# Performance work log

Measured on AMD Instinct MI355X. Metric: run time of the kernel, lower is better.

## Reference

```python
import jax, jax.numpy as jnp
import numpy as np

B = 32          # num graphs
N = 4096        # nodes per graph (temporal length after reshape)
TOT = B * N     # 131072 total nodes
F = 64          # num_features
HS = 128        # hidden_dim_s
RS = 32         # rank_s
HT = 128        # hidden_dim_t
RT = 32         # rank_t
E = 1048576     # num edges


def setup_inputs() -> dict:
    key = jax.random.key(0)
    ks = jax.random.split(key, 20)
    x = jax.random.normal(ks[0], (TOT, F), jnp.float32)
    edge_index = jax.random.randint(ks[1], (2, E), 0, TOT, dtype=jnp.int64)
    batch = jnp.repeat(jnp.arange(B, dtype=jnp.int64), N)

    def lin(k, fan_in, fan_out):
        s = 1.0 / np.sqrt(fan_in)
        return jax.random.uniform(k, (fan_in, fan_out), jnp.float32, -s, s)

    def conv(k, cout, cin):
        s = 1.0 / np.sqrt(cin * 3)
        return jax.random.uniform(k, (cout, cin, 3), jnp.float32, -s, s)

    return {
        "x": x, "edge_index": edge_index, "batch": batch,
        "W1": lin(ks[2], F, HS), "b1": jnp.zeros((HS,), jnp.float32),
        "W2": lin(ks[3], HS, RS), "b2": jnp.zeros((RS,), jnp.float32),
        "W3": lin(ks[4], RS, HS), "b3": jnp.zeros((HS,), jnp.float32),
        "tW1": conv(ks[5], HT, HS), "tb1": jnp.zeros((HT,), jnp.float32),
        "tW2": conv(ks[6], RT, HT), "tb2": jnp.zeros((RT,), jnp.float32),
        "tW3": conv(ks[7], HT, RT), "tb3": jnp.zeros((HT,), jnp.float32),
        "Wpi": lin(ks[8], HT, 1), "bpi": jnp.zeros((1,), jnp.float32),
        "Wn": lin(ks[9], HT, 1), "bn": jnp.zeros((1,), jnp.float32),
        "Wp": lin(ks[10], HT, 1), "bp": jnp.zeros((1,), jnp.float32),
    }


def reference(x, edge_index, batch,
              W1, b1, W2, b2, W3, b3,
              tW1, tb1, tW2, tb2, tW3, tb3,
              Wpi, bpi, Wn, bn, Wp, bp):
    src, dst = edge_index[0], edge_index[1]
    n = x.shape[0]

    # GCN symmetric normalization with added self-loops (PyG GCNConv default)
    deg = jnp.zeros((n,), x.dtype).at[dst].add(1.0) + 1.0  # +1 self-loop
    dinv = jax.lax.rsqrt(deg)
    enorm = dinv[src] * dinv[dst]       # [E] edge normalization
    snorm = dinv * dinv                 # [n] self-loop normalization

    def gcn(h, W, b):
        h = h @ W                                            # [n, out]
        agg = jnp.zeros_like(h).at[dst].add(h[src] * enorm[:, None])
        return agg + h * snorm[:, None] + b

    xs = jax.nn.relu(gcn(x, W1, b1))
    xs = jax.nn.relu(gcn(xs, W2, b2))
    xs = jax.nn.relu(gcn(xs, W3, b3))    # [TOT, HS]

    num_graphs = B  # == batch.max() + 1 (batch is repeat(arange(B), N))
    xs = xs.reshape(num_graphs, -1, xs.shape[-1]).transpose(0, 2, 1)  # [B, HS, N]

    def conv1d(z, w, bias):
        y = jax.lax.conv_general_dilated(
            z, w, window_strides=(1,), padding=((1, 1),),
            dimension_numbers=("NCH", "OIH", "NCH"))
        return y + bias[None, :, None]

    xt = jax.nn.relu(conv1d(xs, tW1, tb1))
    xt = jax.nn.relu(conv1d(xt, tW2, tb2))
    xt = jax.nn.relu(conv1d(xt, tW3, tb3))                   # [B, HT, N]

    xt = xt.transpose(0, 2, 1).reshape(-1, xt.shape[1])      # [TOT, HT]

    pi = jax.nn.sigmoid(xt @ Wpi + bpi)
    nb = jax.nn.softplus(xt @ Wn + bn)
    p = jax.nn.sigmoid(xt @ Wp + bp)
    return (pi, nb, p)
```

## Files before the change

kernel.cpp:

```cpp
#include <hip/hip_runtime.h>
#include <cmath>

constexpr int TOT = 131072;
constexpr int NE  = 1048576;
constexpr int NMASK = 4095;

constexpr int NB   = 512;
constexpr int DPB  = 256;
constexpr int BCAP = 4096;
constexpr int EPB  = 2048;

typedef __attribute__((ext_vector_type(8))) short bf16x8;
typedef __attribute__((ext_vector_type(4))) float f32x4;

__device__ inline float bf2f(unsigned int u16) {
    union { unsigned int i; float f; } x; x.i = u16 << 16; return x.f;
}
__device__ inline unsigned short f2bf(float f) {
    union { float f; unsigned int i; } x; x.f = f;
    unsigned int r = (x.i + 0x7fffu + ((x.i >> 16) & 1u)) >> 16;
    return (unsigned short)r;
}
__device__ inline void unpack8(uint4 v, float* f) {
    f[0] = bf2f(v.x & 0xffffu); f[1] = bf2f(v.x >> 16);
    f[2] = bf2f(v.y & 0xffffu); f[3] = bf2f(v.y >> 16);
    f[4] = bf2f(v.z & 0xffffu); f[5] = bf2f(v.z >> 16);
    f[6] = bf2f(v.w & 0xffffu); f[7] = bf2f(v.w >> 16);
}
__device__ inline uint4 pack8(const float* f) {
    uint4 v;
    v.x = (unsigned)f2bf(f[0]) | ((unsigned)f2bf(f[1]) << 16);
    v.y = (unsigned)f2bf(f[2]) | ((unsigned)f2bf(f[3]) << 16);
    v.z = (unsigned)f2bf(f[4]) | ((unsigned)f2bf(f[5]) << 16);
    v.w = (unsigned)f2bf(f[6]) | ((unsigned)f2bf(f[7]) << 16);
    return v;
}

__device__ inline void pack_one(const float* __restrict__ w, unsigned short* __restrict__ wp,
                                int CIN, int COUT, int taps, int idx) {
    int j = idx & 7;
    int L = (idx >> 3) & 63;
    int f = idx >> 9;
    int NT = COUT >> 4;
    int kc = f / NT, nt = f - kc * NT;
    int k = kc * 32 + (L >> 4) * 8 + j;
    int n = nt * 16 + (L & 15);
    float v;
    if (taps == 1) v = w[k * COUT + n];
    else { int t = k / CIN, c = k - t * CIN; v = w[(n * CIN + c) * 3 + t]; }
    wp[idx] = f2bf(v);
}

struct PackArgs {
    const float *W1, *W2, *W3, *tW1, *tW2, *tW3;
    unsigned short *g1, *g2, *g3, *c1, *c2, *c3;
};
__global__ __launch_bounds__(256) void k_part(const int* __restrict__ src,
                                              const int* __restrict__ dst,
                                              int* __restrict__ gcur,
                                              unsigned* __restrict__ buf,
                                              PackArgs pa) {
    __shared__ int hist[NB];
    __shared__ int cbase[NB];
    __shared__ int lcur[NB];
    const int tid = threadIdx.x;
    const int e0 = blockIdx.x * EPB;

    for (int b = tid; b < NB; b += 256) hist[b] = 0;
    __syncthreads();
    for (int i = tid; i < EPB; i += 256)
        atomicAdd(&hist[dst[e0 + i] >> 8], 1);
    __syncthreads();
    for (int b = tid; b < NB; b += 256) {
        int c = hist[b];
        cbase[b] = (c > 0) ? atomicAdd(&gcur[b * 32], c) : 0;
        lcur[b] = 0;
    }
    __syncthreads();
    for (int i = tid; i < EPB; i += 256) {
        int e = e0 + i;
        int d = dst[e];
        int b = d >> 8;
        int p = atomicAdd(&lcur[b], 1);
        buf[b * BCAP + cbase[b] + p] = ((unsigned)src[e] << 8) | (unsigned)(d & 255);
    }
    int gid = blockIdx.x * 256 + tid;
    if      (gid <  8192) pack_one(pa.W1,  pa.g1, 64, 128, 1, gid);
    else if (gid < 12288) pack_one(pa.W2,  pa.g2, 128, 32, 1, gid - 8192);
    else if (gid < 16384) pack_one(pa.W3,  pa.g3, 32, 128, 1, gid - 12288);
    else if (gid < 65536) pack_one(pa.tW1, pa.c1, 128, 128, 3, gid - 16384);
    else if (gid < 77824) pack_one(pa.tW2, pa.c2, 128, 32, 3, gid - 65536);
    else if (gid < 90112) pack_one(pa.tW3, pa.c3, 32, 128, 3, gid - 77824);
}

__global__ __launch_bounds__(256) void k_bcsr(const unsigned* __restrict__ buf,
                                              const int* __restrict__ gcur,
                                              int* __restrict__ adj,
                                              int2* __restrict__ rse,
                                              float* __restrict__ dinv,
                                              const float4* __restrict__ x,
                                              uint4* __restrict__ xsc) {
    __shared__ int cnt[DPB];
    __shared__ int start[DPB];
    __shared__ int cur[DPB];
    __shared__ int sc[DPB];
    const int b = blockIdx.x;
    const int tid = threadIdx.x;
    cnt[tid] = 0;
    __syncthreads();
    const int n = gcur[b * 32];
    const unsigned* eb = buf + b * BCAP;
    for (int i = tid; i < n; i += 256)
        atomicAdd(&cnt[eb[i] & 255u], 1);
    __syncthreads();
    int v = cnt[tid];
    sc[tid] = v;
    __syncthreads();
    for (int off = 1; off < 256; off <<= 1) {
        int a = sc[tid];
        int p = (tid >= off) ? sc[tid - off] : 0;
        __syncthreads();
        sc[tid] = a + p;
        __syncthreads();
    }
    int st = sc[tid] - v;
    start[tid] = st;
    cur[tid] = 0;
    int d = (b << 8) + tid;
    rse[d] = make_int2(b * BCAP + st, v);
    dinv[d] = rsqrtf((float)v + 1.0f);
    __syncthreads();
    for (int i = tid; i < n; i += 256) {
        unsigned w = eb[i];
        int dl = (int)(w & 255u);
        int p = atomicAdd(&cur[dl], 1);
        adj[b * BCAP + start[dl] + p] = (int)(w >> 8);
    }
    for (int i = tid; i < DPB * 8; i += 256) {
        int rl = i >> 3;
        int t = (b << 11) + i;
        float dv = rsqrtf((float)cnt[rl] + 1.0f);
        float4 v0 = x[t * 2], v1 = x[t * 2 + 1];
        float f[8] = { v0.x * dv, v0.y * dv, v0.z * dv, v0.w * dv,
                       v1.x * dv, v1.y * dv, v1.z * dv, v1.w * dv };
        xsc[t] = pack8(f);
    }
}

template<int LC>
__global__ __launch_bounds__(256) void k_gcsr(const uint4* __restrict__ xs,
                                              const int* __restrict__ adj,
                                              const int2* __restrict__ rse,
                                              const float* __restrict__ dinv,
                                              const float* __restrict__ bias,
                                              uint4* __restrict__ out) {
    int t = blockIdx.x * 256 + threadIdx.x;
    int d = t >> LC;
    int g = t & ((1 << LC) - 1);
    float a[8];
    unpack8(xs[t], a);
    int2 se = rse[d];
    int e = se.x, end = se.x + se.y;
    for (; e + 4 <= end; e += 4) {
        int s0 = adj[e], s1 = adj[e + 1], s2 = adj[e + 2], s3 = adj[e + 3];
        uint4 v0 = xs[(s0 << LC) + g];
        uint4 v1 = xs[(s1 << LC) + g];
        uint4 v2 = xs[(s2 << LC) + g];
        uint4 v3 = xs[(s3 << LC) + g];
        float f[8];
        unpack8(v0, f);
#pragma unroll
        for (int j = 0; j < 8; ++j) a[j] += f[j];
        unpack8(v1, f);
#pragma unroll
        for (int j = 0; j < 8; ++j) a[j] += f[j];
        unpack8(v2, f);
#pragma unroll
        for (int j = 0; j < 8; ++j) a[j] += f[j];
        unpack8(v3, f);
#pragma unroll
        for (int j = 0; j < 8; ++j) a[j] += f[j];
    }
    for (; e < end; ++e) {
        float f[8];
        unpack8(xs[(adj[e] << LC) + g], f);
#pragma unroll
        for (int j = 0; j < 8; ++j) a[j] += f[j];
    }
    float dv = dinv[d];
#pragma unroll
    for (int j = 0; j < 8; ++j)
        a[j] = fmaxf(fmaf(a[j], dv, bias[g * 8 + j]), 0.0f) * dv;
    out[t] = pack8(a);
}

__global__ __launch_bounds__(256) void k_gmm2(const uint4* __restrict__ xs,
                                              const int* __restrict__ adj,
                                              const int2* __restrict__ rse,
                                              const float* __restrict__ dinv,
                                              const bf16x8* __restrict__ wp1,
                                              const float* __restrict__ b1,
                                              const bf16x8* __restrict__ wp2,
                                              unsigned short* __restrict__ y) {
    constexpr int CIN = 64;
    constexpr int ROWS = 64;
    constexpr int SC  = CIN + 8;
    constexpr int SCH = 144;
    constexpr int NV = CIN / 8;
    constexpr int VPT = NV / 4;
    __shared__ __attribute__((aligned(16))) unsigned short tile1[ROWS * SC];
    __shared__ __attribute__((aligned(16))) unsigned short h1t[ROWS * SCH];

    const int R0 = blockIdx.x * ROWS;
    const int tid = threadIdx.x;

    {
        int r = R0 + (tid >> 2);
        int g = tid & 3;
        const uint4* base = xs + (long)r * NV + g * VPT;
        float a[VPT * 8];
#pragma unroll
        for (int v = 0; v < VPT; ++v) unpack8(base[v], a + v * 8);
        int2 se = rse[r];
        int e = se.x, end = se.x + se.y;
        for (; e + 4 <= end; e += 4) {
            int s0 = adj[e], s1 = adj[e + 1], s2 = adj[e + 2], s3 = adj[e + 3];
            const uint4* p0 = xs + (long)s0 * NV + g * VPT;
            const uint4* p1 = xs + (long)s1 * NV + g * VPT;
            const uint4* p2 = xs + (long)s2 * NV + g * VPT;
            const uint4* p3 = xs + (long)s3 * NV + g * VPT;
            uint4 v0[VPT], v1[VPT], v2[VPT], v3[VPT];
#pragma unroll
            for (int v = 0; v < VPT; ++v) { v0[v] = p0[v]; v1[v] = p1[v]; v2[v] = p2[v]; v3[v] = p3[v]; }
            float f[VPT * 8];
#pragma unroll
            for (int v = 0; v < VPT; ++v) unpack8(v0[v], f + v * 8);
#pragma unroll
            for (int j = 0; j < VPT * 8; ++j) a[j] += f[j];
#pragma unroll
            for (int v = 0; v < VPT; ++v) unpack8(v1[v], f + v * 8);
#pragma unroll
            for (int j = 0; j < VPT * 8; ++j) a[j] += f[j];
#pragma unroll
            for (int v = 0; v < VPT; ++v) unpack8(v2[v], f + v * 8);
#pragma unroll
            for (int j = 0; j < VPT * 8; ++j) a[j] += f[j];
#pragma unroll
            for (int v = 0; v < VPT; ++v) unpack8(v3[v], f + v * 8);
#pragma unroll
            for (int j = 0; j < VPT * 8; ++j) a[j] += f[j];
        }
        for (; e < end; ++e) {
            const uint4* p0 = xs + (long)adj[e] * NV + g * VPT;
            float f[VPT * 8];
#pragma unroll
            for (int v = 0; v < VPT; ++v) unpack8(p0[v], f + v * 8);
#pragma unroll
            for (int j = 0; j < VPT * 8; ++j) a[j] += f[j];
        }
        float dv = dinv[r];
#pragma unroll
        for (int j = 0; j < VPT * 8; ++j) a[j] *= dv;
        uint4* dst4 = (uint4*)(tile1 + (tid >> 2) * SC + g * VPT * 8);
#pragma unroll
        for (int v = 0; v < VPT; ++v) dst4[v] = pack8(a + v * 8);
    }
    __syncthreads();

    const int lane = tid & 63;
    const int w = tid >> 6;
    const int l16 = lane & 15;
    const int q = lane >> 4;

    {
        f32x4 acc[4][2];
#pragma unroll
        for (int wm = 0; wm < 4; ++wm)
#pragma unroll
            for (int nt = 0; nt < 2; ++nt) acc[wm][nt] = (f32x4){0.f, 0.f, 0.f, 0.f};
        const bf16x8* wpl = wp1 + lane;
        const int nt0 = w * 2;
#pragma unroll
        for (int kc = 0; kc < 2; ++kc) {
            bf16x8 a[4];
#pragma unroll
            for (int wm = 0; wm < 4; ++wm)
                a[wm] = *(const bf16x8*)(tile1 + (wm * 16 + l16) * SC + kc * 32 + q * 8);
            bf16x8 b[2];
#pragma unroll
            for (int nt = 0; nt < 2; ++nt)
                b[nt] = wpl[(kc * 8 + nt0 + nt) * 64];
#pragma unroll
            for (int wm = 0; wm < 4; ++wm)
#pragma unroll
                for (int nt = 0; nt < 2; ++nt)
                    acc[wm][nt] = __builtin_amdgcn_mfma_f32_16x16x32_bf16(a[wm], b[nt], acc[wm][nt], 0, 0, 0);
        }
#pragma unroll
        for (int wm = 0; wm < 4; ++wm) {
#pragma unroll
            for (int nt = 0; nt < 2; ++nt) {
                int col = w * 32 + nt * 16 + l16;
                float bi = b1[col];
#pragma unroll
                for (int r = 0; r < 4; ++r) {
                    int row = wm * 16 + q * 4 + r;
                    h1t[row * SCH + col] = f2bf(fmaxf(acc[wm][nt][r] + bi, 0.0f));
                }
            }
        }
    }
    __syncthreads();

    {
        const int colbase = (w & 1) * 16;
        const int rowbase = (w >> 1) * 32;
        const int nt0 = colbase >> 4;
        f32x4 acc[2];
#pragma unroll
        for (int wm = 0; wm < 2; ++wm) acc[wm] = (f32x4){0.f, 0.f, 0.f, 0.f};
        const bf16x8* wpl = wp2 + lane;
#pragma unroll
        for (int kc = 0; kc < 4; ++kc) {
            bf16x8 a[2];
#pragma unroll
            for (int wm = 0; wm < 2; ++wm)
                a[wm] = *(const bf16x8*)(h1t + (rowbase + wm * 16 + l16) * SCH + kc * 32 + q * 8);
            bf16x8 b = wpl[(kc * 2 + nt0) * 64];
#pragma unroll
            for (int wm = 0; wm < 2; ++wm)
                acc[wm] = __builtin_amdgcn_mfma_f32_16x16x32_bf16(a[wm], b, acc[wm], 0, 0, 0);
        }
#pragma unroll
        for (int wm = 0; wm < 2; ++wm) {
            int col = colbase + l16;
#pragma unroll
            for (int r = 0; r < 4; ++r) {
                int row = R0 + rowbase + wm * 16 + q * 4 + r;
                float v = acc[wm][r] * dinv[row];
                y[(long)row * 32 + col] = f2bf(v);
            }
        }
    }
}

template<int CIN, bool RELU>
__global__ __launch_bounds__(256) void k_gmm(const uint4* __restrict__ xs,
                                             const int* __restrict__ adj,
                                             const int2* __restrict__ rse,
                                             const float* __restrict__ dinv,
                                             const bf16x8* __restrict__ wp,
                                             const float* __restrict__ bias,
                                             unsigned short* __restrict__ y) {
    constexpr int COUT = 128;
    constexpr int ROWS = 64;
    constexpr int SC = CIN + 8;
    constexpr int NV = CIN / 8;
    constexpr int VPT = NV / 4;
    constexpr int NK = CIN / 32;
    constexpr int NT = COUT / 16;
    constexpr int WN = 2, WM = 4;
    __shared__ __attribute__((aligned(16))) unsigned short tile[ROWS * SC];

    const int R0 = blockIdx.x * ROWS;
    const int tid = threadIdx.x;

    {
        int r = R0 + (tid >> 2);
        int g = tid & 3;
        const uint4* base = xs + (long)r * NV + g * VPT;
        float a[VPT * 8];
#pragma unroll
        for (int v = 0; v < VPT; ++v) unpack8(base[v], a + v * 8);
        int2 se = rse[r];
        int e = se.x, end = se.x + se.y;
        for (; e + 4 <= end; e += 4) {
            int s0 = adj[e], s1 = adj[e + 1], s2 = adj[e + 2], s3 = adj[e + 3];
            const uint4* p0 = xs + (long)s0 * NV + g * VPT;
            const uint4* p1 = xs + (long)s1 * NV + g * VPT;
            const uint4* p2 = xs + (long)s2 * NV + g * VPT;
            const uint4* p3 = xs + (long)s3 * NV + g * VPT;
            uint4 v0[VPT], v1[VPT], v2[VPT], v3[VPT];
#pragma unroll
            for (int v = 0; v < VPT; ++v) { v0[v] = p0[v]; v1[v] = p1[v]; v2[v] = p2[v]; v3[v] = p3[v]; }
            float f[VPT * 8];
#pragma unroll
            for (int v = 0; v < VPT; ++v) unpack8(v0[v], f + v * 8);
#pragma unroll
            for (int j = 0; j < VPT * 8; ++j) a[j] += f[j];
#pragma unroll
            for (int v = 0; v < VPT; ++v) unpack8(v1[v], f + v * 8);
#pragma unroll
            for (int j = 0; j < VPT * 8; ++j) a[j] += f[j];
#pragma unroll
            for (int v = 0; v < VPT; ++v) unpack8(v2[v], f + v * 8);
#pragma unroll
            for (int j = 0; j < VPT * 8; ++j) a[j] += f[j];
#pragma unroll
            for (int v = 0; v < VPT; ++v) unpack8(v3[v], f + v * 8);
#pragma unroll
            for (int j = 0; j < VPT * 8; ++j) a[j] += f[j];
        }
        for (; e < end; ++e) {
            const uint4* p0 = xs + (long)adj[e] * NV + g * VPT;
            float f[VPT * 8];
#pragma unroll
            for (int v = 0; v < VPT; ++v) unpack8(p0[v], f + v * 8);
#pragma unroll
            for (int j = 0; j < VPT * 8; ++j) a[j] += f[j];
        }
        float dv = dinv[r];
#pragma unroll
        for (int j = 0; j < VPT * 8; ++j) a[j] *= dv;
        uint4* dst4 = (uint4*)(tile + (tid >> 2) * SC + g * VPT * 8);
#pragma unroll
        for (int v = 0; v < VPT; ++v) dst4[v] = pack8(a + v * 8);
    }
    __syncthreads();

    const int lane = threadIdx.x & 63;
    const int w = threadIdx.x >> 6;
    const int l16 = lane & 15;
    const int q = lane >> 4;
    const int colbase = w * 32;
    const int nt0 = colbase >> 4;

    f32x4 acc[WM][WN];
#pragma unroll
    for (int wm = 0; wm < WM; ++wm)
#pragma unroll
        for (int nt = 0; nt < WN; ++nt) acc[wm][nt] = (f32x4){0.f, 0.f, 0.f, 0.f};

    const bf16x8* __restrict__ wpl = wp + lane;

#pragma unroll
    for (int kc = 0; kc < NK; ++kc) {
        bf16x8 a[WM];
#pragma unroll
        for (int wm = 0; wm < WM; ++wm)
            a[wm] = *(const bf16x8*)(tile + (wm * 16 + l16) * SC + kc * 32 + q * 8);
        bf16x8 b[WN];
#pragma unroll
        for (int nt = 0; nt < WN; ++nt)
            b[nt] = wpl[(kc * NT + nt0 + nt) * 64];
#pragma unroll
        for (int wm = 0; wm < WM; ++wm)
#pragma unroll
            for (int nt = 0; nt < WN; ++nt)
                acc[wm][nt] = __builtin_amdgcn_mfma_f32_16x16x32_bf16(a[wm], b[nt], acc[wm][nt], 0, 0, 0);
    }

#pragma unroll
    for (int wm = 0; wm < WM; ++wm) {
#pragma unroll
        for (int nt = 0; nt < WN; ++nt) {
            int col = colbase + nt * 16 + l16;
            float bi = bias[col];
#pragma unroll
            for (int r = 0; r < 4; ++r) {
                int row = R0 + wm * 16 + q * 4 + r;
                float v = acc[wm][nt][r] + bi;
                if (RELU) v = fmaxf(v, 0.0f);
                y[(long)row * COUT + col] = f2bf(v);
            }
        }
    }
}

template<int CIN, int COUT, int TAPS, bool RELU, bool BIAS, bool SOUT>
__global__ __launch_bounds__(256) void k_mm(const unsigned short* __restrict__ x,
                                            const bf16x8* __restrict__ wp,
                                            const float* __restrict__ bias,
                                            const float* __restrict__ dinv,
                                            unsigned short* __restrict__ y) {
    constexpr int ROWS = 64;
    constexpr int HALO = (TAPS == 3) ? 1 : 0;
    constexpr int TR = ROWS + 2 * HALO;
    constexpr int SC = CIN + 8;
    constexpr int NCH = CIN / 32;
    constexpr int NK = TAPS * NCH;
    constexpr int NT = COUT / 16;
    constexpr int WN = (COUT == 128) ? 2 : 1;
    constexpr int WM = (COUT == 128) ? 4 : 2;
    __shared__ __attribute__((aligned(16))) unsigned short tile[TR * SC];

    const int R0 = blockIdx.x * ROWS;
    const int n0 = R0 & NMASK; (void)n0;

    constexpr int NLD = TR * (CIN / 8);
    for (int idx = threadIdx.x; idx < NLD; idx += 256) {
        int tr = idx / (CIN / 8);
        int c8 = idx - tr * (CIN / 8);
        int ro = tr - HALO;
        bool valid = true;
        if (TAPS == 3) {
            if (ro < 0) valid = (n0 > 0);
            else if (ro >= ROWS) valid = (n0 + ROWS < 4096);
        }
        uint4 v = make_uint4(0, 0, 0, 0);
        if (valid) v = *(const uint4*)(x + (long)(R0 + ro) * CIN + c8 * 8);
        *(uint4*)(tile + tr * SC + c8 * 8) = v;
    }
    __syncthreads();

    const int lane = threadIdx.x & 63;
    const int w = threadIdx.x >> 6;
    const int l16 = lane & 15;
    const int q = lane >> 4;
    const int colbase = (COUT == 128) ? w * 32 : (w & 1) * 16;
    const int rowbase = (COUT == 128) ? 0 : (w >> 1) * 32;
    const int nt0 = colbase >> 4;

    f32x4 acc[WM][WN];
#pragma unroll
    for (int wm = 0; wm < WM; ++wm)
#pragma unroll
        for (int nt = 0; nt < WN; ++nt) acc[wm][nt] = (f32x4){0.f, 0.f, 0.f, 0.f};

    const bf16x8* __restrict__ wpl = wp + lane;

#pragma unroll
    for (int kc = 0; kc < NK; ++kc) {
        const int tap = (TAPS == 3) ? (kc / NCH) : 0;
        const int ch  = (TAPS == 3) ? (kc - tap * NCH) : kc;
        bf16x8 a[WM];
#pragma unroll
        for (int wm = 0; wm < WM; ++wm)
            a[wm] = *(const bf16x8*)(tile + (rowbase + wm * 16 + l16 + tap) * SC + ch * 32 + q * 8);
        bf16x8 b[WN];
#pragma unroll
        for (int nt = 0; nt < WN; ++nt)
            b[nt] = wpl[(kc * NT + nt0 + nt) * 64];
#pragma unroll
        for (int wm = 0; wm < WM; ++wm)
#pragma unroll
            for (int nt = 0; nt < WN; ++nt)
                acc[wm][nt] = __builtin_amdgcn_mfma_f32_16x16x32_bf16(a[wm], b[nt], acc[wm][nt], 0, 0, 0);
    }

#pragma unroll
    for (int wm = 0; wm < WM; ++wm) {
#pragma unroll
        for (int nt = 0; nt < WN; ++nt) {
            int col = colbase + nt * 16 + l16;
            float bi = BIAS ? bias[col] : 0.0f;
#pragma unroll
            for (int r = 0; r < 4; ++r) {
                int row = R0 + rowbase + wm * 16 + q * 4 + r;
                float v = acc[wm][nt][r] + bi;
                if (RELU) v = fmaxf(v, 0.0f);
                if (SOUT) v *= dinv[row];
                y[(long)row * COUT + col] = f2bf(v);
            }
        }
    }
}

__global__ __launch_bounds__(256) void k_c23_heads(
    const unsigned short* __restrict__ x,
    const bf16x8* __restrict__ wp2, const float* __restrict__ tb2,
    const bf16x8* __restrict__ wp3, const float* __restrict__ tb3,
    const float* __restrict__ Wpi, const float* __restrict__ bpi,
    const float* __restrict__ Wn,  const float* __restrict__ bn,
    const float* __restrict__ Wp,  const float* __restrict__ bp,
    float* __restrict__ out) {
    constexpr int SC1 = 136;
    constexpr int SC2 = 40;
    __shared__ __attribute__((aligned(16))) unsigned short shl[82 * 136 + 66 * 40];
    unsigned short* c1  = shl;
    unsigned short* c2  = shl + 82 * 136;
    unsigned short* xts = shl;

    const int R0 = blockIdx.x * 64;
    const int n0 = R0 & NMASK;
    const int tid = threadIdx.x;

    for (int i = tid; i < 82 * 16; i += 256) {
        int r = i >> 4;
        int c8 = i & 15;
        int n = n0 - 2 + r;
        uint4 v = make_uint4(0, 0, 0, 0);
        if (n >= 0 && n < 4096)
            v = *(const uint4*)(x + (long)(R0 - 2 + r) * 128 + c8 * 8);
        *(uint4*)(c1 + r * SC1 + c8 * 8) = v;
    }
    __syncthreads();

    const int lane = tid & 63;
    const int w = tid >> 6;
    const int l16 = lane & 15;
    const int q = lane >> 4;

    for (int rt = w; rt < 5; rt += 4) {
        f32x4 acc[2];
#pragma unroll
        for (int nt = 0; nt < 2; ++nt) acc[nt] = (f32x4){0.f, 0.f, 0.f, 0.f};
        const bf16x8* wpl = wp2 + lane;
#pragma unroll
        for (int kc = 0; kc < 12; ++kc) {
            int tap = kc >> 2, ch = kc & 3;
            bf16x8 a = *(const bf16x8*)(c1 + (16 * rt + l16 + tap) * SC1 + ch * 32 + q * 8);
            bf16x8 b0 = wpl[(kc * 2 + 0) * 64];
            bf16x8 b1 = wpl[(kc * 2 + 1) * 64];
            acc[0] = __builtin_amdgcn_mfma_f32_16x16x32_bf16(a, b0, acc[0], 0, 0, 0);
            acc[1] = __builtin_amdgcn_mfma_f32_16x16x32_bf16(a, b1, acc[1], 0, 0, 0);
        }
#pragma unroll
        for (int nt = 0; nt < 2; ++nt) {
            int col = nt * 16 + l16;
            float bi = tb2[col];
#pragma unroll
            for (int r = 0; r < 4; ++r) {
                int idx = 16 * rt + q * 4 + r;
                if (idx < 66) {
                    int n = n0 - 1 + idx;
                    unsigned short v = 0;
                    if (n >= 0 && n < 4096)
                        v = f2bf(fmaxf(acc[nt][r] + bi, 0.0f));
                    c2[idx * SC2 + col] = v;
                }
            }
        }
    }
    __syncthreads();

    {
        f32x4 acc[4][2];
#pragma unroll
        for (int rt = 0; rt < 4; ++rt)
#pragma unroll
            for (int nt = 0; nt < 2; ++nt) acc[rt][nt] = (f32x4){0.f, 0.f, 0.f, 0.f};
        const bf16x8* wpl = wp3 + lane;
#pragma unroll
        for (int kc = 0; kc < 3; ++kc) {
            bf16x8 a[4];
#pragma unroll
            for (int rt = 0; rt < 4; ++rt)
                a[rt] = *(const bf16x8*)(c2 + (16 * rt + l16 + kc) * SC2 + q * 8);
            bf16x8 b[2];
#pragma unroll
            for (int nt = 0; nt < 2; ++nt)
                b[nt] = wpl[(kc * 8 + 2 * w + nt) * 64];
#pragma unroll
            for (int rt = 0; rt < 4; ++rt)
#pragma unroll
                for (int nt = 0; nt < 2; ++nt)
                    acc[rt][nt] = __builtin_amdgcn_mfma_f32_16x16x32_bf16(a[rt], b[nt], acc[rt][nt], 0, 0, 0);
        }
#pragma unroll
        for (int rt = 0; rt < 4; ++rt) {
#pragma unroll
            for (int nt = 0; nt < 2; ++nt) {
                int col = w * 32 + nt * 16 + l16;
                float bi = tb3[col];
#pragma unroll
                for (int r = 0; r < 4; ++r) {
                    int row = 16 * rt + q * 4 + r;
                    xts[row * 130 + col] = f2bf(fmaxf(acc[rt][nt][r] + bi, 0.0f));
                }
            }
        }
    }
    __syncthreads();

    if (tid < 192) {
        int h = tid >> 6;
        int row = tid & 63;
        const float* Wh = (h == 0) ? Wpi : (h == 1) ? Wn : Wp;
        float s = 0.0f;
        const unsigned short* xr = xts + row * 130;
#pragma unroll
        for (int c2i = 0; c2i < 64; ++c2i) {
            unsigned u = *(const unsigned*)(xr + c2i * 2);
            s = fmaf(bf2f(u & 0xffffu), Wh[c2i * 2], s);
            s = fmaf(bf2f(u >> 16), Wh[c2i * 2 + 1], s);
        }
        float bb = (h == 0) ? bpi[0] : (h == 1) ? bn[0] : bp[0];
        float z = s + bb;
        float o;
        if (h == 1) o = (z > 20.0f) ? z : log1pf(expf(z));
        else        o = 1.0f / (1.0f + expf(-z));
        out[h * TOT + R0 + row] = o;
    }
}

extern "C" void kernel_launch(void* const* d_in, const int* in_sizes, int n_in,
                              void* d_out, int out_size, void* d_ws, size_t ws_size,
                              hipStream_t stream) {
    const float* x   = (const float*)d_in[0];
    const int*   ei  = (const int*)d_in[1];
    const int*   src = ei;
    const int*   dst = ei + NE;
    const float* W1 = (const float*)d_in[3];
    const float* b1 = (const float*)d_in[4];
    const float* W2 = (const float*)d_in[5];
    const float* b2 = (const float*)d_in[6];
    const float* W3 = (const float*)d_in[7];
    const float* b3 = (const float*)d_in[8];
    const float* tW1 = (const float*)d_in[9];
    const float* tb1 = (const float*)d_in[10];
    const float* tW2 = (const float*)d_in[11];
    const float* tb2 = (const float*)d_in[12];
    const float* tW3 = (const float*)d_in[13];
    const float* tb3 = (const float*)d_in[14];
    const float* Wpi = (const float*)d_in[15];
    const float* bpi = (const float*)d_in[16];
    const float* Wn  = (const float*)d_in[17];
    const float* bn  = (const float*)d_in[18];
    const float* Wp  = (const float*)d_in[19];
    const float* bp  = (const float*)d_in[20];

    char* ws = (char*)d_ws;
    float* dinv = (float*)(ws + (0ull << 20));
    int*   gcur = (int*)  (ws + (1ull << 20));
    int2*  rse  = (int2*) (ws + (1ull << 20) + (256 << 10));
    unsigned short* wpG1 = (unsigned short*)(ws + (3ull << 20));
    unsigned short* wpG2 = (unsigned short*)(ws + (3ull << 20) + (128 << 10));
    unsigned short* wpG3 = (unsigned short*)(ws + (3ull << 20) + (256 << 10));
    unsigned short* wpC1 = (unsigned short*)(ws + (3ull << 20) + (384 << 10));
    unsigned short* wpC2 = (unsigned short*)(ws + (3ull << 20) + (512 << 10));
    unsigned short* wpC3 = (unsigned short*)(ws + (3ull << 20) + (640 << 10));
    unsigned* buf = (unsigned*)(ws + (4ull << 20));
    int* adj = (int*)(ws + (12ull << 20));
    unsigned short* Xa = (unsigned short*)(ws + (24ull  << 20));
    unsigned short* Xb = (unsigned short*)(ws + (44ull  << 20));
    unsigned short* Xc = (unsigned short*)(ws + (80ull  << 20));
    unsigned short* Xd = (unsigned short*)(ws + (116ull << 20));
    unsigned short* Xe = (unsigned short*)(ws + (128ull << 20));

    hipMemsetAsync(gcur, 0, NB * 32 * sizeof(int), stream);

    PackArgs pa = { W1, W2, W3, tW1, tW2, tW3, wpG1, wpG2, wpG3, wpC1, wpC2, wpC3 };
    k_part<<<NE / EPB, 256, 0, stream>>>(src, dst, gcur, buf, pa);
    k_bcsr<<<NB, 256, 0, stream>>>(buf, gcur, adj, rse, dinv, (const float4*)x, (uint4*)Xa);

    k_gmm2<<<TOT / 64, 256, 0, stream>>>((const uint4*)Xa, adj, rse, dinv,
                                         (const bf16x8*)wpG1, b1, (const bf16x8*)wpG2, Xd);

    k_gcsr<2><<<TOT * 4 / 256, 256, 0, stream>>>((const uint4*)Xd, adj, rse, dinv,
                                                 b2, (uint4*)Xe);

    k_gmm<32, true><<<TOT / 64, 256, 0, stream>>>((const uint4*)Xe, adj, rse, dinv,
                                                  (const bf16x8*)wpG3, b3, Xb);

    k_mm<128, 128, 3, true, true, false>
        <<<TOT / 64, 256, 0, stream>>>(Xb, (const bf16x8*)wpC1, tb1, nullptr, Xc);

    k_c23_heads<<<TOT / 64, 256, 0, stream>>>(Xc,
                                              (const bf16x8*)wpC2, tb2,
                                              (const bf16x8*)wpC3, tb3,
                                              Wpi, bpi, Wn, bn, Wp, bp, (float*)d_out);
}
```

Baseline: 276.7 us.

## Fuse third GCN layer with first temporal conv using halo recompute

Merges the layer-3 GCN aggregation+matmul kernel with the first 3-tap temporal conv kernel. Each block aggregates 66 rows (64 plus a one-row halo on each side), computes the 128-wide GCN output into shared memory, then runs the conv from LDS, so the 128-channel intermediate never goes to global memory. This removes one kernel launch and a full bf16 write and read of a TOT x 128 tensor. In exchange it recomputes the halo-row gathers and matmuls and uses more LDS per block.

Result: no change. 277.2 us (+0.2%).

```diff
diff --git a/kernel.cpp b/kernel.cpp
--- a/kernel.cpp
+++ b/kernel.cpp
@@ -344,213 +344,147 @@
     }
 }
 
-template<int CIN, bool RELU>
-__global__ __launch_bounds__(256) void k_gmm(const uint4* __restrict__ xs,
-                                             const int* __restrict__ adj,
-                                             const int2* __restrict__ rse,
-                                             const float* __restrict__ dinv,
-                                             const bf16x8* __restrict__ wp,
-                                             const float* __restrict__ bias,
-                                             unsigned short* __restrict__ y) {
-    constexpr int COUT = 128;
-    constexpr int ROWS = 64;
-    constexpr int SC = CIN + 8;
-    constexpr int NV = CIN / 8;
-    constexpr int VPT = NV / 4;
-    constexpr int NK = CIN / 32;
-    constexpr int NT = COUT / 16;
-    constexpr int WN = 2, WM = 4;
-    __shared__ __attribute__((aligned(16))) unsigned short tile[ROWS * SC];
-
-    const int R0 = blockIdx.x * ROWS;
+__global__ __launch_bounds__(256) void k_gmc1(
+    const uint4* __restrict__ xs,
+    const int* __restrict__ adj,
+    const int2* __restrict__ rse,
+    const float* __restrict__ dinv,
+    const bf16x8* __restrict__ wp3, const float* __restrict__ b3,
+    const bf16x8* __restrict__ wpc1, const float* __restrict__ tb1,
+    unsigned short* __restrict__ y) {
+    constexpr int SCA = 40;
+    constexpr int SCH = 144;
+    __shared__ __attribute__((aligned(16))) unsigned short atile[80 * SCA];
+    __shared__ __attribute__((aligned(16))) unsigned short h3t[66 * SCH];
+
+    const int R0 = blockIdx.x * 64;
+    const int n0 = R0 & NMASK;
     const int tid = threadIdx.x;
 
-    {
-        int r = R0 + (tid >> 2);
-        int g = tid & 3;
-        const uint4* base = xs + (long)r * NV + g * VPT;
-        float a[VPT * 8];
-#pragma unroll
-        for (int v = 0; v < VPT; ++v) unpack8(base[v], a + v * 8);
-        int2 se = rse[r];
-        int e = se.x, end = se.x + se.y;
-        for (; e + 4 <= end; e += 4) {
-            int s0 = adj[e], s1 = adj[e + 1], s2 = adj[e + 2], s3 = adj[e + 3];
-            const uint4* p0 = xs + (long)s0 * NV + g * VPT;
-            const uint4* p1 = xs + (long)s1 * NV + g * VPT;
-            const uint4* p2 = xs + (long)s2 * NV + g * VPT;
-            const uint4* p3 = xs + (long)s3 * NV + g * VPT;
-            uint4 v0[VPT], v1[VPT], v2[VPT], v3[VPT];
-#pragma unroll
-            for (int v = 0; v < VPT; ++v) { v0[v] = p0[v]; v1[v] = p1[v]; v2[v] = p2[v]; v3[v] = p3[v]; }
-            float f[VPT * 8];
-#pragma unroll
-            for (int v = 0; v < VPT; ++v) unpack8(v0[v], f + v * 8);
-#pragma unroll
-            for (int j = 0; j < VPT * 8; ++j) a[j] += f[j];
-#pragma unroll
-            for (int v = 0; v < VPT; ++v) unpack8(v1[v], f + v * 8);
-#pragma unroll
-            for (int j = 0; j < VPT * 8; ++j) a[j] += f[j];
-#pragma unroll
-            for (int v = 0; v < VPT; ++v) unpack8(v2[v], f + v * 8);
-#pragma unroll
-            for (int j = 0; j < VPT * 8; ++j) a[j] += f[j];
-#pragma unroll
-            for (int v = 0; v < VPT; ++v) unpack8(v3[v], f + v * 8);
-#pragma unroll
-            for (int j = 0; j < VPT * 8; ++j) a[j] += f[j];
-        }
-        for (; e < end; ++e) {
-            const uint4* p0 = xs + (long)adj[e] * NV + g * VPT;
-            float f[VPT * 8];
-#pragma unroll
-            for (int v = 0; v < VPT; ++v) unpack8(p0[v], f + v * 8);
-#pragma unroll
-            for (int j = 0; j < VPT * 8; ++j) a[j] += f[j];
-        }
-        float dv = dinv[r];
-#pragma unroll
-        for (int j = 0; j < VPT * 8; ++j) a[j] *= dv;
-        uint4* dst4 = (uint4*)(tile + (tid >> 2) * SC + g * VPT * 8);
-#pragma unroll
-        for (int v = 0; v < VPT; ++v) dst4[v] = pack8(a + v * 8);
-    }
-    __syncthreads();
-
-    const int lane = threadIdx.x & 63;
-    const int w = threadIdx.x >> 6;
+    for (int i = tid; i < 14 * 5; i += 256) {
+        int r = 66 + i / 5, c = i % 5;
+        *(uint4*)(atile + r * SCA + c * 8) = make_uint4(0, 0, 0, 0);
+    }
+
+    for (int it = tid; it < 66 * 4; it += 256) {
+        int rr = it >> 2, g = it & 3;
+        int n = n0 - 1 + rr;
+        float a[8] = {0.f, 0.f, 0.f, 0.f, 0.f, 0.f, 0.f, 0.f};
+        if (n >= 0 && n < 4096) {
+            int gr = R0 - 1 + rr;
+            unpack8(xs[gr * 4 + g], a);
+            int2 se = rse[gr];
+            int e = se.x, end = se.x + se.y;
+            for (; e + 4 <= end; e += 4) {
+                int s0 = adj[e], s1 = adj[e + 1], s2 = adj[e + 2], s3 = adj[e + 3];
+                uint4 v0 = xs[(s0 << 2) + g];
+                uint4 v1 = xs[(s1 << 2) + g];
+                uint4 v2 = xs[(s2 << 2) + g];
+                uint4 v3 = xs[(s3 << 2) + g];
+                float f[8];
+                unpack8(v0, f);
+#pragma unroll
+                for (int j = 0; j < 8; ++j) a[j] += f[j];
+                unpack8(v1, f);
+#pragma unroll
+                for (int j = 0; j < 8; ++j) a[j] += f[j];
+                unpack8(v2, f);
+#pragma unroll
+                for (int j = 0; j < 8; ++j) a[j] += f[j];
+                unpack8(v3, f);
+#pragma unroll
+                for (int j = 0; j < 8; ++j) a[j] += f[j];
+            }
+            for (; e < end; ++e) {
+                float f[8];
+                unpack8(xs[(adj[e] << 2) + g], f);
+#pragma unroll
+                for (int j = 0; j < 8; ++j) a[j] += f[j];
+            }
+            float dv = dinv[gr];
+#pragma unroll
+            for (int j = 0; j < 8; ++j) a[j] *= dv;
+        }
+        *(uint4*)(atile + rr * SCA + g * 8) = pack8(a);
+    }
+    __syncthreads();
+
+    const int lane = tid & 63;
+    const int w = tid >> 6;
     const int l16 = lane & 15;
     const int q = lane >> 4;
-    const int colbase = w * 32;
-    const int nt0 = colbase >> 4;
-
-    f32x4 acc[WM][WN];
-#pragma unroll
-    for (int wm = 0; wm < WM; ++wm)
-#pragma unroll
-        for (int nt = 0; nt < WN; ++nt) acc[wm][nt] = (f32x4){0.f, 0.f, 0.f, 0.f};
-
-    const bf16x8* __restrict__ wpl = wp + lane;
-
-#pragma unroll
-    for (int kc = 0; kc < NK; ++kc) {
-        bf16x8 a[WM];
-#pragma unroll
-        for (int wm = 0; wm < WM; ++wm)
-            a[wm] = *(const bf16x8*)(tile + (wm * 16 + l16) * SC + kc * 32 + q * 8);
-        bf16x8 b[WN];
-#pragma unroll
-        for (int nt = 0; nt < WN; ++nt)
-            b[nt] = wpl[(kc * NT + nt0 + nt) * 64];
-#pragma unroll
-        for (int wm = 0; wm < WM; ++wm)
-#pragma unroll
-            for (int nt = 0; nt < WN; ++nt)
-                acc[wm][nt] = __builtin_amdgcn_mfma_f32_16x16x32_bf16(a[wm], b[nt], acc[wm][nt], 0, 0, 0);
-    }
-
-#pragma unroll
-    for (int wm = 0; wm < WM; ++wm) {
-#pragma unroll
-        for (int nt = 0; nt < WN; ++nt) {
-            int col = colbase + nt * 16 + l16;
-            float bi = bias[col];
-#pragma unroll
-            for (int r = 0; r < 4; ++r) {
-                int row = R0 + wm * 16 + q * 4 + r;
-                float v = acc[wm][nt][r] + bi;
-                if (RELU) v = fmaxf(v, 0.0f);
-                y[(long)row * COUT + col] = f2bf(v);
-            }
-        }
-    }
-}
-
-template<int CIN, int COUT, int TAPS, bool RELU, bool BIAS, bool SOUT>
-__global__ __launch_bounds__(256) void k_mm(const unsigned short* __restrict__ x,
-                                            const bf16x8* __restrict__ wp,
-                                            const float* __restrict__ bias,
-                                            const float* __restrict__ dinv,
-                                            unsigned short* __restrict__ y) {
-    constexpr int ROWS = 64;
-    constexpr int HALO = (TAPS == 3) ? 1 : 0;
-    constexpr int TR = ROWS + 2 * HALO;
-    constexpr int SC = CIN + 8;
-    constexpr int NCH = CIN / 32;
-    constexpr int NK = TAPS * NCH;
-    constexpr int NT = COUT / 16;
-    constexpr int WN = (COUT == 128) ? 2 : 1;
-    constexpr int WM = (COUT == 128) ? 4 : 2;
-    __shared__ __attribute__((aligned(16))) unsigned short tile[TR * SC];
-
-    const int R0 = blockIdx.x * ROWS;
-    const int n0 = R0 & NMASK; (void)n0;
-
-    constexpr int NLD = TR * (CIN / 8);
-    for (int idx = threadIdx.x; idx < NLD; idx += 256) {
-        int tr = idx / (CIN / 8);
-        int c8 = idx - tr * (CIN / 8);
-        int ro = tr - HALO;
-        bool valid = true;
-        if (TAPS == 3) {
-            if (ro < 0) valid = (n0 > 0);
-            else if (ro >= ROWS) valid = (n0 + ROWS < 4096);
-        }
-        uint4 v = make_uint4(0, 0, 0, 0);
-        if (valid) v = *(const uint4*)(x + (long)(R0 + ro) * CIN + c8 * 8);
-        *(uint4*)(tile + tr * SC + c8 * 8) = v;
-    }
-    __syncthreads();
-
-    const int lane = threadIdx.x & 63;
-    const int w = threadIdx.x >> 6;
-    const int l16 = lane & 15;
-    const int q = lane >> 4;
-    const int colbase = (COUT == 128) ? w * 32 : (w & 1) * 16;
-    const int rowbase = (COUT == 128) ? 0 : (w >> 1) * 32;
-    const int nt0 = colbase >> 4;
-
-    f32x4 acc[WM][WN];
-#pragma unroll
-    for (int wm = 0; wm < WM; ++wm)
-#pragma unroll
-        for (int nt = 0; nt < WN; ++nt) acc[wm][nt] = (f32x4){0.f, 0.f, 0.f, 0.f};
-
-    const bf16x8* __restrict__ wpl = wp + lane;
-
-#pragma unroll
-    for (int kc = 0; kc < NK; ++kc) {
-        const int tap = (TAPS == 3) ? (kc / NCH) : 0;
-        const int ch  = (TAPS == 3) ? (kc - tap * NCH) : kc;
-        bf16x8 a[WM];
-#pragma unroll
-        for (int wm = 0; wm < WM; ++wm)
-            a[wm] = *(const bf16x8*)(tile + (rowbase + wm * 16 + l16 + tap) * SC + ch * 32 + q * 8);
-        bf16x8 b[WN];
-#pragma unroll
-        for (int nt = 0; nt < WN; ++nt)
-            b[nt] = wpl[(kc * NT + nt0 + nt) * 64];
-#pragma unroll
-        for (int wm = 0; wm < WM; ++wm)
-#pragma unroll
-            for (int nt = 0; nt < WN; ++nt)
-                acc[wm][nt] = __builtin_amdgcn_mfma_f32_16x16x32_bf16(a[wm], b[nt], acc[wm][nt], 0, 0, 0);
-    }
-
-#pragma unroll
-    for (int wm = 0; wm < WM; ++wm) {
-#pragma unroll
-        for (int nt = 0; nt < WN; ++nt) {
-            int col = colbase + nt * 16 + l16;
-            float bi = BIAS ? bias[col] : 0.0f;
-#pragma unroll
-            for (int r = 0; r < 4; ++r) {
-                int row = R0 + rowbase + wm * 16 + q * 4 + r;
-                float v = acc[wm][nt][r] + bi;
-                if (RELU) v = fmaxf(v, 0.0f);
-                if (SOUT) v *= dinv[row];
-                y[(long)row * COUT + col] = f2bf(v);
+
+    {
+        f32x4 acc[5][2];
+#pragma unroll
+        for (int rt = 0; rt < 5; ++rt)
+#pragma unroll
+            for (int nt = 0; nt < 2; ++nt) acc[rt][nt] = (f32x4){0.f, 0.f, 0.f, 0.f};
+        const bf16x8* wpl = wp3 + lane;
+        bf16x8 b[2];
+        b[0] = wpl[(w * 2 + 0) * 64];
+        b[1] = wpl[(w * 2 + 1) * 64];
+#pragma unroll
+        for (int rt = 0; rt < 5; ++rt) {
+            bf16x8 a = *(const bf16x8*)(atile + (16 * rt + l16) * SCA + q * 8);
+            acc[rt][0] = __builtin_amdgcn_mfma_f32_16x16x32_bf16(a, b[0], acc[rt][0], 0, 0, 0);
+            acc[rt][1] = __builtin_amdgcn_mfma_f32_16x16x32_bf16(a, b[1], acc[rt][1], 0, 0, 0);
+        }
+#pragma unroll
+        for (int rt = 0; rt < 5; ++rt) {
+#pragma unroll
+            for (int nt = 0; nt < 2; ++nt) {
+                int col = w * 32 + nt * 16 + l16;
+                float bi = b3[col];
+#pragma unroll
+                for (int r = 0; r < 4; ++r) {
+                    int rr = 16 * rt + q * 4 + r;
+                    if (rr < 66) {
+                        int n = n0 - 1 + rr;
+                        unsigned short v = 0;
+                        if (n >= 0 && n < 4096)
+                            v = f2bf(fmaxf(acc[rt][nt][r] + bi, 0.0f));
+                        h3t[rr * SCH + col] = v;
+                    }
+                }
+            }
+        }
+    }
+    __syncthreads();
+
+    {
+        f32x4 acc[4][2];
+#pragma unroll
+        for (int rt = 0; rt < 4; ++rt)
+#pragma unroll
+            for (int nt = 0; nt < 2; ++nt) acc[rt][nt] = (f32x4){0.f, 0.f, 0.f, 0.f};
+        const bf16x8* wpl = wpc1 + lane;
+#pragma unroll
+        for (int kc = 0; kc < 12; ++kc) {
+            int tap = kc >> 2, ch = kc & 3;
+            bf16x8 a[4];
+#pragma unroll
+            for (int rt = 0; rt < 4; ++rt)
+                a[rt] = *(const bf16x8*)(h3t + (16 * rt + l16 + tap) * SCH + ch * 32 + q * 8);
+            bf16x8 b0 = wpl[(kc * 8 + 2 * w + 0) * 64];
+            bf16x8 b1 = wpl[(kc * 8 + 2 * w + 1) * 64];
+#pragma unroll
+            for (int rt = 0; rt < 4; ++rt) {
+                acc[rt][0] = __builtin_amdgcn_mfma_f32_16x16x32_bf16(a[rt], b0, acc[rt][0], 0, 0, 0);
+                acc[rt][1] = __builtin_amdgcn_mfma_f32_16x16x32_bf16(a[rt], b1, acc[rt][1], 0, 0, 0);
+            }
+        }
+#pragma unroll
+        for (int rt = 0; rt < 4; ++rt) {
+#pragma unroll
+            for (int nt = 0; nt < 2; ++nt) {
+                int col = w * 32 + nt * 16 + l16;
+                float bi = tb1[col];
+#pragma unroll
+                for (int r = 0; r < 4; ++r) {
+                    int row = R0 + 16 * rt + q * 4 + r;
+                    y[(long)row * 128 + col] = f2bf(fmaxf(acc[rt][nt][r] + bi, 0.0f));
+                }
             }
         }
     }
@@ -723,7 +657,6 @@
     unsigned* buf = (unsigned*)(ws + (4ull << 20));
     int* adj = (int*)(ws + (12ull << 20));
     unsigned short* Xa = (unsigned short*)(ws + (24ull  << 20));
-    unsigned short* Xb = (unsigned short*)(ws + (44ull  << 20));
     unsigned short* Xc = (unsigned short*)(ws + (80ull  << 20));
     unsigned short* Xd = (unsigned short*)(ws + (116ull << 20));
     unsigned short* Xe = (unsigned short*)(ws + (128ull << 20));
@@ -740,11 +673,9 @@
     k_gcsr<2><<<TOT * 4 / 256, 256, 0, stream>>>((const uint4*)Xd, adj, rse, dinv,
                                                  b2, (uint4*)Xe);
 
-    k_gmm<32, true><<<TOT / 64, 256, 0, stream>>>((const uint4*)Xe, adj, rse, dinv,
-                                                  (const bf16x8*)wpG3, b3, Xb);
-
-    k_mm<128, 128, 3, true, true, false>
-        <<<TOT / 64, 256, 0, stream>>>(Xb, (const bf16x8*)wpC1, tb1, nullptr, Xc);
+    k_gmc1<<<TOT / 64, 256, 0, stream>>>((const uint4*)Xe, adj, rse, dinv,
+                                         (const bf16x8*)wpG3, b3,
+                                         (const bf16x8*)wpC1, tb1, Xc);
 
     k_c23_heads<<<TOT / 64, 256, 0, stream>>>(Xc,
                                               (const bf16x8*)wpC2, tb2,
```
